# Performance work log

Measured on AMD Instinct MI355X. Metric: run time of the kernel, lower is better.

The kernel has to match this reference:

```python
import jax, jax.numpy as jnp
import numpy as np

N = 100000   # nodes
E = 1600000  # edges (avg degree 16)
D = 64       # feature dim (in_dim)


def setup_inputs() -> dict:
    key = jax.random.key(0)
    k1, k2, k3, k4, k5 = jax.random.split(key, 5)
    h = jax.random.normal(k1, (N, D), dtype=jnp.float32)
    dnorm = jax.random.uniform(k2, (N,), dtype=jnp.float32)  # deg^-1/2 proxy
    # xavier_normal_(gain=1.414) for Linear(2D, 1): std = gain*sqrt(2/(fan_in+fan_out))
    std = 1.414 * np.sqrt(2.0 / (2 * D + 1))
    gate_w = jax.random.normal(k3, (1, 2 * D), dtype=jnp.float32) * std
    gate_b = jnp.zeros((1,), dtype=jnp.float32)
    src = jax.random.randint(k4, (E,), 0, N, dtype=jnp.int32)
    dst = jax.random.randint(k5, (E,), 0, N, dtype=jnp.int32)
    return {"h": h, "dnorm": dnorm, "gate_w": gate_w, "gate_b": gate_b,
            "src": src, "dst": dst}


def reference(h, dnorm, gate_w, gate_b, src, dst):
    # gate(cat[h_dst, h_src]) == h_dst @ W[:, :D].T + h_src @ W[:, D:].T + b
    w_dst = gate_w[0, :D]  # [D]
    w_src = gate_w[0, D:]  # [D]
    h_src = h[src]                                        # [E, D] gather
    g = jnp.tanh(h[dst] @ w_dst + h_src @ w_src + gate_b[0])  # [E]
    e = g * dnorm[dst] * dnorm[src]                       # [E] (dropout p=0 -> identity)
    # u_mul_e + sum: z[v] = sum_{(u->v)} h[u] * e
    z = jax.ops.segment_sum(h_src * e[:, None], dst, num_segments=N)  # [N, D]
    return z
```

## Files before the change

### kernel.cpp

```cpp
#include <hip/hip_runtime.h>
#include <hip/hip_bf16.h>

#define D 64
#define BKT_SHIFT 7
#define BKT_NODES 128
#define NB_CNT 1024
#define DSPLIT_T 1024
#define DSPLIT_E 4096
#define CAP 2560
#define QBINS 512

__device__ __forceinline__ unsigned short f2bf(float x) {
    unsigned u = __float_as_uint(x);
    unsigned r = 0x7fffu + ((u >> 16) & 1u);
    return (unsigned short)((u + r) >> 16);
}

template<bool MAKE_BF16>
__global__ void fal_precompute(const float* __restrict__ h,
                               const float* __restrict__ dnorm,
                               const float* __restrict__ gate_w,
                               const float* __restrict__ gate_b,
                               float2* __restrict__ sd,
                               float2* __restrict__ ss,
                               unsigned short* __restrict__ hb,
                               int* __restrict__ bcursor,
                               int nb, int N) {
    int tid  = threadIdx.x;
    if (blockIdx.x == 0) {
        for (int i = tid; i < nb; i += 256) bcursor[i] = 0;
    }
    int lane = tid & 63;
    int wave = tid >> 6;
    int grp  = lane >> 4;
    int gl   = lane & 15;

    int node = blockIdx.x * 16 + wave * 4 + grp;
    int nc   = node < N ? node : N - 1;

    const float4* h4 = (const float4*)h;
    const float4* w4 = (const float4*)gate_w;

    float4 hv  = h4[nc * 16 + gl];
    float4 wd  = w4[gl];
    float4 wsr = w4[16 + gl];

    if (MAKE_BF16 && node < N) {
        ushort4 p = make_ushort4(f2bf(hv.x), f2bf(hv.y), f2bf(hv.z), f2bf(hv.w));
        *(ushort4*)&hb[(size_t)node * D + gl * 4] = p;
    }

    float a = hv.x * wd.x + hv.y * wd.y + hv.z * wd.z + hv.w * wd.w;
    float b = hv.x * wsr.x + hv.y * wsr.y + hv.z * wsr.z + hv.w * wsr.w;

    for (int off = 1; off < 16; off <<= 1) {
        a += __shfl_xor(a, off, 64);
        b += __shfl_xor(b, off, 64);
    }

    if (gl == 0 && node < N) {
        float dn = dnorm[node];
        sd[node] = make_float2(a + gate_b[0], dn);
        ss[node] = make_float2(b, dn);
    }
}

__global__ __launch_bounds__(DSPLIT_T) void fal_multisplit(
        const int* __restrict__ src,
        const int* __restrict__ dst,
        int* __restrict__ bcursor,
        unsigned* __restrict__ pk_bin,
        int E, int nb) {
    __shared__ int lcount[NB_CNT];
    __shared__ int lscan[NB_CNT];
    __shared__ int gofs[NB_CNT];
    __shared__ int wsum16[16];
    __shared__ unsigned s_pk[DSPLIT_E];
    __shared__ int s_gpos[DSPLIT_E];

    int tid  = threadIdx.x;
    int lane = tid & 63;
    int w    = tid >> 6;
    lcount[tid] = 0;
    __syncthreads();

    int E4 = E >> 2;
    int i4 = blockIdx.x * DSPLIT_T + tid;

    int srcs[4], dsts[4], lr[4];
    bool act = (i4 < E4);
    if (act) {
        int4 s4 = ((const int4*)src)[i4];
        int4 d4 = ((const int4*)dst)[i4];
        srcs[0] = s4.x; srcs[1] = s4.y; srcs[2] = s4.z; srcs[3] = s4.w;
        dsts[0] = d4.x; dsts[1] = d4.y; dsts[2] = d4.z; dsts[3] = d4.w;
        #pragma unroll
        for (int j = 0; j < 4; ++j)
            lr[j] = atomicAdd(&lcount[dsts[j] >> BKT_SHIFT], 1);
    }
    __syncthreads();

    int v = lcount[tid];
    for (int off = 1; off < 64; off <<= 1) {
        int t = __shfl_up(v, off, 64);
        if (lane >= off) v += t;
    }
    if (lane == 63) wsum16[w] = v;
    __syncthreads();
    if (tid < 16) {
        int s = wsum16[tid];
        for (int off = 1; off < 16; off <<= 1) {
            int t = __shfl_up(s, off, 64);
            if (tid >= off) s += t;
        }
        wsum16[tid] = s;
    }
    __syncthreads();
    lscan[tid] = v + (w ? wsum16[w - 1] : 0);

    if (tid < nb) {
        int c = lcount[tid];
        int rel = c ? atomicAdd(&bcursor[tid], c) : 0;
        gofs[tid] = tid * CAP + rel;
    }
    __syncthreads();

    if (act) {
        #pragma unroll
        for (int j = 0; j < 4; ++j) {
            int b = dsts[j] >> BKT_SHIFT;
            int lpos = (lscan[b] - lcount[b]) + lr[j];
            unsigned dl = (unsigned)(dsts[j] & (BKT_NODES - 1));
            s_pk[lpos] = (dl << 20) | (unsigned)srcs[j];
            int gp = gofs[b] + lr[j];
            s_gpos[lpos] = (gp < (b + 1) * CAP) ? gp : -1;
        }
    }
    __syncthreads();

    int total = lscan[NB_CNT - 1];
    for (int t = tid; t < total; t += DSPLIT_T) {
        int g = s_gpos[t];
        if (g >= 0) pk_bin[g] = s_pk[t];
    }
}

#define DRAIN(SEG0, DG, A0, A1, A2, A3, A4, A5, A6, A7) do {             \
    int k_ = 0;                                                          \
    for (; k_ + 2 <= (DG); k_ += 2) {                                    \
        int s0_ = (int)(s_srt[(SEG0) + k_]     & 0xFFFFFu);              \
        int s1_ = (int)(s_srt[(SEG0) + k_ + 1] & 0xFFFFFu);              \
        float e0_ = s_esc[(SEG0) + k_];                                  \
        float e1_ = s_esc[(SEG0) + k_ + 1];                              \
        if constexpr (BF16) {                                            \
            uint4 r0_ = *(const uint4*)&hb[(size_t)s0_ * D + cbase];     \
            uint4 r1_ = *(const uint4*)&hb[(size_t)s1_ * D + cbase];     \
            A0 = fmaf(__uint_as_float(r0_.x << 16),         e0_, A0);    \
            A1 = fmaf(__uint_as_float(r0_.x & 0xffff0000u), e0_, A1);    \
            A2 = fmaf(__uint_as_float(r0_.y << 16),         e0_, A2);    \
            A3 = fmaf(__uint_as_float(r0_.y & 0xffff0000u), e0_, A3);    \
            A4 = fmaf(__uint_as_float(r0_.z << 16),         e0_, A4);    \
            A5 = fmaf(__uint_as_float(r0_.z & 0xffff0000u), e0_, A5);    \
            A6 = fmaf(__uint_as_float(r0_.w << 16),         e0_, A6);    \
            A7 = fmaf(__uint_as_float(r0_.w & 0xffff0000u), e0_, A7);    \
            A0 = fmaf(__uint_as_float(r1_.x << 16),         e1_, A0);    \
            A1 = fmaf(__uint_as_float(r1_.x & 0xffff0000u), e1_, A1);    \
            A2 = fmaf(__uint_as_float(r1_.y << 16),         e1_, A2);    \
            A3 = fmaf(__uint_as_float(r1_.y & 0xffff0000u), e1_, A3);    \
            A4 = fmaf(__uint_as_float(r1_.z << 16),         e1_, A4);    \
            A5 = fmaf(__uint_as_float(r1_.z & 0xffff0000u), e1_, A5);    \
            A6 = fmaf(__uint_as_float(r1_.w << 16),         e1_, A6);    \
            A7 = fmaf(__uint_as_float(r1_.w & 0xffff0000u), e1_, A7);    \
        } else {                                                         \
            const float4* hp0_ = (const float4*)&h[(size_t)s0_ * D + cbase]; \
            const float4* hp1_ = (const float4*)&h[(size_t)s1_ * D + cbase]; \
            float4 q0_ = hp0_[0], q1_ = hp0_[1], q2_ = hp1_[0], q3_ = hp1_[1]; \
            A0 = fmaf(q0_.x, e0_, A0); A1 = fmaf(q0_.y, e0_, A1);        \
            A2 = fmaf(q0_.z, e0_, A2); A3 = fmaf(q0_.w, e0_, A3);        \
            A4 = fmaf(q1_.x, e0_, A4); A5 = fmaf(q1_.y, e0_, A5);        \
            A6 = fmaf(q1_.z, e0_, A6); A7 = fmaf(q1_.w, e0_, A7);        \
            A0 = fmaf(q2_.x, e1_, A0); A1 = fmaf(q2_.y, e1_, A1);        \
            A2 = fmaf(q2_.z, e1_, A2); A3 = fmaf(q2_.w, e1_, A3);        \
            A4 = fmaf(q3_.x, e1_, A4); A5 = fmaf(q3_.y, e1_, A5);        \
            A6 = fmaf(q3_.z, e1_, A6); A7 = fmaf(q3_.w, e1_, A7);        \
        }                                                                \
    }                                                                    \
    if (k_ < (DG)) {                                                     \
        int s0_ = (int)(s_srt[(SEG0) + k_] & 0xFFFFFu);                  \
        float e0_ = s_esc[(SEG0) + k_];                                  \
        if constexpr (BF16) {                                            \
            uint4 r0_ = *(const uint4*)&hb[(size_t)s0_ * D + cbase];     \
            A0 = fmaf(__uint_as_float(r0_.x << 16),         e0_, A0);    \
            A1 = fmaf(__uint_as_float(r0_.x & 0xffff0000u), e0_, A1);    \
            A2 = fmaf(__uint_as_float(r0_.y << 16),         e0_, A2);    \
            A3 = fmaf(__uint_as_float(r0_.y & 0xffff0000u), e0_, A3);    \
            A4 = fmaf(__uint_as_float(r0_.z << 16),         e0_, A4);    \
            A5 = fmaf(__uint_as_float(r0_.z & 0xffff0000u), e0_, A5);    \
            A6 = fmaf(__uint_as_float(r0_.w << 16),         e0_, A6);    \
            A7 = fmaf(__uint_as_float(r0_.w & 0xffff0000u), e0_, A7);    \
        } else {                                                         \
            const float4* hp0_ = (const float4*)&h[(size_t)s0_ * D + cbase]; \
            float4 q0_ = hp0_[0], q1_ = hp0_[1];                         \
            A0 = fmaf(q0_.x, e0_, A0); A1 = fmaf(q0_.y, e0_, A1);        \
            A2 = fmaf(q0_.z, e0_, A2); A3 = fmaf(q0_.w, e0_, A3);        \
            A4 = fmaf(q1_.x, e0_, A4); A5 = fmaf(q1_.y, e0_, A5);        \
            A6 = fmaf(q1_.z, e0_, A6); A7 = fmaf(q1_.w, e0_, A7);        \
        }                                                                \
    }                                                                    \
} while (0)

template<bool BF16>
__global__ __launch_bounds__(512) void fal_bucket_process(
        const float* __restrict__ h,
        const unsigned short* __restrict__ hb,
        const float2* __restrict__ sd,
        const float2* __restrict__ ss,
        const int* __restrict__ bcursor,
        const unsigned* __restrict__ pk_bin,
        float* __restrict__ z, int nfull, int N) {
    __shared__ unsigned s_pk[CAP];
    __shared__ unsigned s_srt[CAP];
    __shared__ float    s_esc[CAP];
    __shared__ float2   sdl[BKT_NODES];
    __shared__ int qhist[QBINS];
    __shared__ int qbase[QBINS];
    __shared__ int qcur[QBINS];
    __shared__ int wsum8[8];

    int bid  = blockIdx.x;
    int tid  = threadIdx.x;
    int lane = tid & 63;
    int w    = tid >> 6;

    int b, h0, is_half;
    if (bid < nfull) { b = bid; h0 = 0; is_half = 0; }
    else {
        int idx = bid - nfull;
        b  = nfull + (idx >> 1);
        h0 = (idx & 1) * 64;
        is_half = 1;
    }

    qhist[tid] = 0;
    if (tid < BKT_NODES) {
        int node = b * BKT_NODES + tid;
        sdl[tid] = (node < N) ? sd[node] : make_float2(0.f, 0.f);
    }
    __syncthreads();

    int cnt = min(bcursor[b], CAP);
    const unsigned* bin = pk_bin + (size_t)b * CAP;

    for (int t = tid; t < cnt; t += 512) {
        unsigned pk = bin[t];
        s_pk[t] = pk;
        int key = (int)(((pk & 0xFFFFFu) >> 15) * 128u + (pk >> 20));
        atomicAdd(&qhist[key], 1);
    }
    __syncthreads();

    int myh = qhist[tid];
    int v = myh;
    for (int off = 1; off < 64; off <<= 1) {
        int t = __shfl_up(v, off, 64);
        if (lane >= off) v += t;
    }
    if (lane == 63) wsum8[w] = v;
    __syncthreads();
    if (tid < 8) {
        int s2 = wsum8[tid];
        for (int off = 1; off < 8; off <<= 1) {
            int t = __shfl_up(s2, off, 64);
            if (tid >= off) s2 += t;
        }
        wsum8[tid] = s2;
    }
    __syncthreads();
    {
        int incl = v + (w ? wsum8[w - 1] : 0);
        qbase[tid] = incl - myh;
        qcur[tid]  = 0;
    }
    __syncthreads();

    for (int t = tid; t < cnt; t += 512) {
        unsigned pk = s_pk[t];
        int dl = (int)(pk >> 20);
        int sn = (int)(pk & 0xFFFFFu);
        int key = (sn >> 15) * 128 + dl;
        int r  = atomicAdd(&qcur[key], 1);
        float2 sv = ss[sn];
        float2 dv = sdl[dl];
        float esc = tanhf(dv.x + sv.x) * dv.y * sv.y;
        int p = qbase[key] + r;
        s_srt[p] = pk;
        s_esc[p] = esc;
    }
    __syncthreads();

    int oct   = tid >> 3;
    int sdim  = tid & 7;
    int cbase = sdim * 8;

    float a0 = 0.f, a1 = 0.f, a2 = 0.f, a3 = 0.f;
    float a4 = 0.f, a5 = 0.f, a6 = 0.f, a7 = 0.f;
    float b0 = 0.f, b1 = 0.f, b2 = 0.f, b3 = 0.f;
    float b4 = 0.f, b5 = 0.f, b6 = 0.f, b7 = 0.f;

    if (!is_half) {
        for (int q = 0; q < 4; ++q) {
            int keyA = q * 128 + oct;
            DRAIN(qbase[keyA], qhist[keyA], a0, a1, a2, a3, a4, a5, a6, a7);
            int keyB = q * 128 + oct + 64;
            DRAIN(qbase[keyB], qhist[keyB], b0, b1, b2, b3, b4, b5, b6, b7);
            __syncthreads();
        }
        int nodeA = b * BKT_NODES + oct;
        if (nodeA < N) {
            float4* zp = (float4*)&z[(size_t)nodeA * D + cbase];
            zp[0] = make_float4(a0, a1, a2, a3);
            zp[1] = make_float4(a4, a5, a6, a7);
        }
        int nodeB = b * BKT_NODES + oct + 64;
        if (nodeB < N) {
            float4* zp = (float4*)&z[(size_t)nodeB * D + cbase];
            zp[0] = make_float4(b0, b1, b2, b3);
            zp[1] = make_float4(b4, b5, b6, b7);
        }
    } else {
        for (int q = 0; q < 4; ++q) {
            int keyA = q * 128 + h0 + oct;
            DRAIN(qbase[keyA], qhist[keyA], a0, a1, a2, a3, a4, a5, a6, a7);
            __syncthreads();
        }
        int nodeA = b * BKT_NODES + h0 + oct;
        if (nodeA < N) {
            float4* zp = (float4*)&z[(size_t)nodeA * D + cbase];
            zp[0] = make_float4(a0, a1, a2, a3);
            zp[1] = make_float4(a4, a5, a6, a7);
        }
    }
}

extern "C" void kernel_launch(void* const* d_in, const int* in_sizes, int n_in,
                              void* d_out, int out_size, void* d_ws, size_t ws_size,
                              hipStream_t stream) {
    const float* h      = (const float*)d_in[0];
    const float* dnorm  = (const float*)d_in[1];
    const float* gate_w = (const float*)d_in[2];
    const float* gate_b = (const float*)d_in[3];
    const int*   src    = (const int*)d_in[4];
    const int*   dst    = (const int*)d_in[5];
    float*       z      = (float*)d_out;

    int N  = in_sizes[1];
    int E  = in_sizes[4];
    int nb = (N + BKT_NODES - 1) >> BKT_SHIFT;

    char* ws0 = (char*)d_ws;
    size_t off = 0;
    auto alloc = [&](size_t bytes) {
        char* p = ws0 + off;
        off += (bytes + 15) & ~(size_t)15;
        return p;
    };
    float2*   sd      = (float2*)alloc((size_t)N * sizeof(float2));
    float2*   ss      = (float2*)alloc((size_t)N * sizeof(float2));
    int*      bcursor = (int*)alloc((size_t)nb * sizeof(int));
    unsigned* pk_bin  = (unsigned*)alloc((size_t)nb * CAP * sizeof(unsigned));
    unsigned short* hb = (unsigned short*)(ws0 + off);
    size_t need_with_hb = off + (size_t)N * D * sizeof(unsigned short);
    bool use_bf16 = (ws_size >= need_with_hb);

    int nfull = nb & ~255;
    int grid3 = nfull + 2 * (nb - nfull);

    if (use_bf16)
        fal_precompute<true><<<(N + 15) / 16, 256, 0, stream>>>(
            h, dnorm, gate_w, gate_b, sd, ss, hb, bcursor, nb, N);
    else
        fal_precompute<false><<<(N + 15) / 16, 256, 0, stream>>>(
            h, dnorm, gate_w, gate_b, sd, ss, hb, bcursor, nb, N);

    fal_multisplit<<<(E + DSPLIT_E - 1) / DSPLIT_E, DSPLIT_T, 0, stream>>>(
        src, dst, bcursor, pk_bin, E, nb);

    if (use_bf16)
        fal_bucket_process<true><<<grid3, 512, 0, stream>>>(
            h, hb, sd, ss, bcursor, pk_bin, z, nfull, N);
    else
        fal_bucket_process<false><<<grid3, 512, 0, stream>>>(
            h, hb, sd, ss, bcursor, pk_bin, z, nfull, N);
}
```

Before: 150.3 us.

## Fuse precompute and multisplit into one launch, drop per-quarter barriers

Merges the per-node gate precompute and the edge bucketing multisplit into a single 1024-thread kernel, with block ranges selecting the role. The bcursor reset moves to a hipMemsetAsync so the split blocks no longer depend on the precompute kernel. This removes one kernel launch and lets both independent stages overlap on the GPU. It also deletes the __syncthreads inside the drain loops of bucket_process, which is only safe if the shared buffers read there are not rewritten between quarters. The precompute blocks now run at 1024 threads and carry the large shared-memory footprint of the split path, which may lower their occupancy.

```diff
diff --git a/kernel.cpp b/kernel.cpp
--- a/kernel.cpp
+++ b/kernel.cpp
@@ -17,131 +17,126 @@
 }
 
 template<bool MAKE_BF16>
-__global__ void fal_precompute(const float* __restrict__ h,
-                               const float* __restrict__ dnorm,
-                               const float* __restrict__ gate_w,
-                               const float* __restrict__ gate_b,
-                               float2* __restrict__ sd,
-                               float2* __restrict__ ss,
-                               unsigned short* __restrict__ hb,
-                               int* __restrict__ bcursor,
-                               int nb, int N) {
-    int tid  = threadIdx.x;
-    if (blockIdx.x == 0) {
-        for (int i = tid; i < nb; i += 256) bcursor[i] = 0;
-    }
-    int lane = tid & 63;
-    int wave = tid >> 6;
-    int grp  = lane >> 4;
-    int gl   = lane & 15;
-
-    int node = blockIdx.x * 16 + wave * 4 + grp;
-    int nc   = node < N ? node : N - 1;
-
-    const float4* h4 = (const float4*)h;
-    const float4* w4 = (const float4*)gate_w;
-
-    float4 hv  = h4[nc * 16 + gl];
-    float4 wd  = w4[gl];
-    float4 wsr = w4[16 + gl];
-
-    if (MAKE_BF16 && node < N) {
-        ushort4 p = make_ushort4(f2bf(hv.x), f2bf(hv.y), f2bf(hv.z), f2bf(hv.w));
-        *(ushort4*)&hb[(size_t)node * D + gl * 4] = p;
-    }
-
-    float a = hv.x * wd.x + hv.y * wd.y + hv.z * wd.z + hv.w * wd.w;
-    float b = hv.x * wsr.x + hv.y * wsr.y + hv.z * wsr.z + hv.w * wsr.w;
-
-    for (int off = 1; off < 16; off <<= 1) {
-        a += __shfl_xor(a, off, 64);
-        b += __shfl_xor(b, off, 64);
-    }
-
-    if (gl == 0 && node < N) {
-        float dn = dnorm[node];
-        sd[node] = make_float2(a + gate_b[0], dn);
-        ss[node] = make_float2(b, dn);
-    }
-}
-
-__global__ __launch_bounds__(DSPLIT_T) void fal_multisplit(
+__global__ __launch_bounds__(1024) void fal_pre_split(
+        const float* __restrict__ h,
+        const float* __restrict__ dnorm,
+        const float* __restrict__ gate_w,
+        const float* __restrict__ gate_b,
+        float2* __restrict__ sd,
+        float2* __restrict__ ss,
+        unsigned short* __restrict__ hb,
         const int* __restrict__ src,
         const int* __restrict__ dst,
         int* __restrict__ bcursor,
         unsigned* __restrict__ pk_bin,
-        int E, int nb) {
-    __shared__ int lcount[NB_CNT];
-    __shared__ int lscan[NB_CNT];
-    __shared__ int gofs[NB_CNT];
-    __shared__ int wsum16[16];
-    __shared__ unsigned s_pk[DSPLIT_E];
-    __shared__ int s_gpos[DSPLIT_E];
-
+        int E, int nb, int N, int gridB) {
     int tid  = threadIdx.x;
     int lane = tid & 63;
     int w    = tid >> 6;
-    lcount[tid] = 0;
-    __syncthreads();
-
-    int E4 = E >> 2;
-    int i4 = blockIdx.x * DSPLIT_T + tid;
-
-    int srcs[4], dsts[4], lr[4];
-    bool act = (i4 < E4);
-    if (act) {
-        int4 s4 = ((const int4*)src)[i4];
-        int4 d4 = ((const int4*)dst)[i4];
-        srcs[0] = s4.x; srcs[1] = s4.y; srcs[2] = s4.z; srcs[3] = s4.w;
-        dsts[0] = d4.x; dsts[1] = d4.y; dsts[2] = d4.z; dsts[3] = d4.w;
-        #pragma unroll
-        for (int j = 0; j < 4; ++j)
-            lr[j] = atomicAdd(&lcount[dsts[j] >> BKT_SHIFT], 1);
-    }
-    __syncthreads();
-
-    int v = lcount[tid];
-    for (int off = 1; off < 64; off <<= 1) {
-        int t = __shfl_up(v, off, 64);
-        if (lane >= off) v += t;
-    }
-    if (lane == 63) wsum16[w] = v;
-    __syncthreads();
-    if (tid < 16) {
-        int s = wsum16[tid];
+
+    if ((int)blockIdx.x < gridB) {
+        __shared__ int lcount[NB_CNT];
+        __shared__ int lscan[NB_CNT];
+        __shared__ int gofs[NB_CNT];
+        __shared__ int wsum16[16];
+        __shared__ unsigned s_pk[DSPLIT_E];
+        __shared__ int s_gpos[DSPLIT_E];
+
+        lcount[tid] = 0;
+        __syncthreads();
+
+        int E4 = E >> 2;
+        int i4 = blockIdx.x * DSPLIT_T + tid;
+
+        int srcs[4], dsts[4], lr[4];
+        bool act = (i4 < E4);
+        if (act) {
+            int4 s4 = ((const int4*)src)[i4];
+            int4 d4 = ((const int4*)dst)[i4];
+            srcs[0] = s4.x; srcs[1] = s4.y; srcs[2] = s4.z; srcs[3] = s4.w;
+            dsts[0] = d4.x; dsts[1] = d4.y; dsts[2] = d4.z; dsts[3] = d4.w;
+            #pragma unroll
+            for (int j = 0; j < 4; ++j)
+                lr[j] = atomicAdd(&lcount[dsts[j] >> BKT_SHIFT], 1);
+        }
+        __syncthreads();
+
+        int v = lcount[tid];
+        for (int off = 1; off < 64; off <<= 1) {
+            int t = __shfl_up(v, off, 64);
+            if (lane >= off) v += t;
+        }
+        if (lane == 63) wsum16[w] = v;
+        __syncthreads();
+        if (tid < 16) {
+            int s = wsum16[tid];
+            for (int off = 1; off < 16; off <<= 1) {
+                int t = __shfl_up(s, off, 64);
+                if (tid >= off) s += t;
+            }
+            wsum16[tid] = s;
+        }
+        __syncthreads();
+        lscan[tid] = v + (w ? wsum16[w - 1] : 0);
+
+        if (tid < nb) {
+            int c = lcount[tid];
+            int rel = c ? atomicAdd(&bcursor[tid], c) : 0;
+            gofs[tid] = tid * CAP + rel;
+        }
+        __syncthreads();
+
+        if (act) {
+            #pragma unroll
+            for (int j = 0; j < 4; ++j) {
+                int b = dsts[j] >> BKT_SHIFT;
+                int lpos = (lscan[b] - lcount[b]) + lr[j];
+                unsigned dl = (unsigned)(dsts[j] & (BKT_NODES - 1));
+                s_pk[lpos] = (dl << 20) | (unsigned)srcs[j];
+                int gp = gofs[b] + lr[j];
+                s_gpos[lpos] = (gp < (b + 1) * CAP) ? gp : -1;
+            }
+        }
+        __syncthreads();
+
+        int total = lscan[NB_CNT - 1];
+        for (int t = tid; t < total; t += DSPLIT_T) {
+            int g = s_gpos[t];
+            if (g >= 0) pk_bin[g] = s_pk[t];
+        }
+    } else {
+        int bid  = blockIdx.x - gridB;
+        int grp  = lane >> 4;
+        int gl   = lane & 15;
+
+        int node = bid * 64 + w * 4 + grp;
+        int nc   = node < N ? node : N - 1;
+
+        const float4* h4 = (const float4*)h;
+        const float4* w4 = (const float4*)gate_w;
+
+        float4 hv  = h4[nc * 16 + gl];
+        float4 wd  = w4[gl];
+        float4 wsr = w4[16 + gl];
+
+        if (MAKE_BF16 && node < N) {
+            ushort4 p = make_ushort4(f2bf(hv.x), f2bf(hv.y), f2bf(hv.z), f2bf(hv.w));
+            *(ushort4*)&hb[(size_t)node * D + gl * 4] = p;
+        }
+
+        float a = hv.x * wd.x + hv.y * wd.y + hv.z * wd.z + hv.w * wd.w;
+        float b = hv.x * wsr.x + hv.y * wsr.y + hv.z * wsr.z + hv.w * wsr.w;
+
         for (int off = 1; off < 16; off <<= 1) {
-            int t = __shfl_up(s, off, 64);
-            if (tid >= off) s += t;
-        }
-        wsum16[tid] = s;
-    }
-    __syncthreads();
-    lscan[tid] = v + (w ? wsum16[w - 1] : 0);
-
-    if (tid < nb) {
-        int c = lcount[tid];
-        int rel = c ? atomicAdd(&bcursor[tid], c) : 0;
-        gofs[tid] = tid * CAP + rel;
-    }
-    __syncthreads();
-
-    if (act) {
-        #pragma unroll
-        for (int j = 0; j < 4; ++j) {
-            int b = dsts[j] >> BKT_SHIFT;
-            int lpos = (lscan[b] - lcount[b]) + lr[j];
-            unsigned dl = (unsigned)(dsts[j] & (BKT_NODES - 1));
-            s_pk[lpos] = (dl << 20) | (unsigned)srcs[j];
-            int gp = gofs[b] + lr[j];
-            s_gpos[lpos] = (gp < (b + 1) * CAP) ? gp : -1;
-        }
-    }
-    __syncthreads();
-
-    int total = lscan[NB_CNT - 1];
-    for (int t = tid; t < total; t += DSPLIT_T) {
-        int g = s_gpos[t];
-        if (g >= 0) pk_bin[g] = s_pk[t];
+            a += __shfl_xor(a, off, 64);
+            b += __shfl_xor(b, off, 64);
+        }
+
+        if (gl == 0 && node < N) {
+            float dn = dnorm[node];
+            sd[node] = make_float2(a + gate_b[0], dn);
+            ss[node] = make_float2(b, dn);
+        }
     }
 }
 
@@ -313,7 +308,6 @@
             DRAIN(qbase[keyA], qhist[keyA], a0, a1, a2, a3, a4, a5, a6, a7);
             int keyB = q * 128 + oct + 64;
             DRAIN(qbase[keyB], qhist[keyB], b0, b1, b2, b3, b4, b5, b6, b7);
-            __syncthreads();
         }
         int nodeA = b * BKT_NODES + oct;
         if (nodeA < N) {
@@ -331,7 +325,6 @@
         for (int q = 0; q < 4; ++q) {
             int keyA = q * 128 + h0 + oct;
             DRAIN(qbase[keyA], qhist[keyA], a0, a1, a2, a3, a4, a5, a6, a7);
-            __syncthreads();
         }
         int nodeA = b * BKT_NODES + h0 + oct;
         if (nodeA < N) {
@@ -372,18 +365,21 @@
     size_t need_with_hb = off + (size_t)N * D * sizeof(unsigned short);
     bool use_bf16 = (ws_size >= need_with_hb);
 
+    int gridB = (E + DSPLIT_E - 1) / DSPLIT_E;
+    int gridA = (N + 63) / 64;
     int nfull = nb & ~255;
     int grid3 = nfull + 2 * (nb - nfull);
 
+    hipMemsetAsync(bcursor, 0, (size_t)nb * sizeof(int), stream);
+
     if (use_bf16)
-        fal_precompute<true><<<(N + 15) / 16, 256, 0, stream>>>(
-            h, dnorm, gate_w, gate_b, sd, ss, hb, bcursor, nb, N);
+        fal_pre_split<true><<<gridB + gridA, 1024, 0, stream>>>(
+            h, dnorm, gate_w, gate_b, sd, ss, hb, src, dst, bcursor, pk_bin,
+            E, nb, N, gridB);
     else
-        fal_precompute<false><<<(N + 15) / 16, 256, 0, stream>>>(
-            h, dnorm, gate_w, gate_b, sd, ss, hb, bcursor, nb, N);
-
-    fal_multisplit<<<(E + DSPLIT_E - 1) / DSPLIT_E, DSPLIT_T, 0, stream>>>(
-        src, dst, bcursor, pk_bin, E, nb);
+        fal_pre_split<false><<<gridB + gridA, 1024, 0, stream>>>(
+            h, dnorm, gate_w, gate_b, sd, ss, hb, src, dst, bcursor, pk_bin,
+            E, nb, N, gridB);
 
     if (use_bf16)
         fal_bucket_process<true><<<grid3, 512, 0, stream>>>(
```

After: 149.7 us. About the same (-0.4%).

## Double edges per multisplit block, split tail buckets into quarters, drop drain syncs

Applied to the files above, without the earlier changes.

The multisplit kernel now handles 8192 edges per block, two int4 loads per thread, which halves the number of blocks and of global bcursor atomics, and makes each bin write burst longer. The shared s_pk/s_gpos arrays grow to 8192 entries, raising LDS use per block and possibly lowering occupancy. Tail buckets in the process kernel are split four ways instead of two, for better load balance on the last partial wave, with only 32 of 64 octets active in those blocks. The __syncthreads inside the drain loops are removed, which looks safe because DRAIN only reads shared data written earlier.

```diff
diff --git a/kernel.cpp b/kernel.cpp
--- a/kernel.cpp
+++ b/kernel.cpp
@@ -6,7 +6,7 @@
 #define BKT_NODES 128
 #define NB_CNT 1024
 #define DSPLIT_T 1024
-#define DSPLIT_E 4096
+#define DSPLIT_E 8192
 #define CAP 2560
 #define QBINS 512
 
@@ -85,19 +85,31 @@
     __syncthreads();
 
     int E4 = E >> 2;
-    int i4 = blockIdx.x * DSPLIT_T + tid;
-
-    int srcs[4], dsts[4], lr[4];
-    bool act = (i4 < E4);
-    if (act) {
-        int4 s4 = ((const int4*)src)[i4];
-        int4 d4 = ((const int4*)dst)[i4];
+    int base4 = blockIdx.x * (DSPLIT_E >> 2);
+    int i4a = base4 + tid;
+    int i4b = base4 + DSPLIT_T + tid;
+
+    int srcs[8], dsts[8], lr[8];
+    bool act_a = (i4a < E4);
+    bool act_b = (i4b < E4);
+    if (act_a) {
+        int4 s4 = ((const int4*)src)[i4a];
+        int4 d4 = ((const int4*)dst)[i4a];
         srcs[0] = s4.x; srcs[1] = s4.y; srcs[2] = s4.z; srcs[3] = s4.w;
         dsts[0] = d4.x; dsts[1] = d4.y; dsts[2] = d4.z; dsts[3] = d4.w;
         #pragma unroll
         for (int j = 0; j < 4; ++j)
             lr[j] = atomicAdd(&lcount[dsts[j] >> BKT_SHIFT], 1);
     }
+    if (act_b) {
+        int4 s4 = ((const int4*)src)[i4b];
+        int4 d4 = ((const int4*)dst)[i4b];
+        srcs[4] = s4.x; srcs[5] = s4.y; srcs[6] = s4.z; srcs[7] = s4.w;
+        dsts[4] = d4.x; dsts[5] = d4.y; dsts[6] = d4.z; dsts[7] = d4.w;
+        #pragma unroll
+        for (int j = 4; j < 8; ++j)
+            lr[j] = atomicAdd(&lcount[dsts[j] >> BKT_SHIFT], 1);
+    }
     __syncthreads();
 
     int v = lcount[tid];
@@ -125,9 +137,20 @@
     }
     __syncthreads();
 
-    if (act) {
+    if (act_a) {
         #pragma unroll
         for (int j = 0; j < 4; ++j) {
+            int b = dsts[j] >> BKT_SHIFT;
+            int lpos = (lscan[b] - lcount[b]) + lr[j];
+            unsigned dl = (unsigned)(dsts[j] & (BKT_NODES - 1));
+            s_pk[lpos] = (dl << 20) | (unsigned)srcs[j];
+            int gp = gofs[b] + lr[j];
+            s_gpos[lpos] = (gp < (b + 1) * CAP) ? gp : -1;
+        }
+    }
+    if (act_b) {
+        #pragma unroll
+        for (int j = 4; j < 8; ++j) {
             int b = dsts[j] >> BKT_SHIFT;
             int lpos = (lscan[b] - lcount[b]) + lr[j];
             unsigned dl = (unsigned)(dsts[j] & (BKT_NODES - 1));
@@ -232,13 +255,13 @@
     int lane = tid & 63;
     int w    = tid >> 6;
 
-    int b, h0, is_half;
-    if (bid < nfull) { b = bid; h0 = 0; is_half = 0; }
+    int b, h0, is_qtr;
+    if (bid < nfull) { b = bid; h0 = 0; is_qtr = 0; }
     else {
         int idx = bid - nfull;
-        b  = nfull + (idx >> 1);
-        h0 = (idx & 1) * 64;
-        is_half = 1;
+        b  = nfull + (idx >> 2);
+        h0 = (idx & 3) * 32;
+        is_qtr = 1;
     }
 
     qhist[tid] = 0;
@@ -307,13 +330,12 @@
     float b0 = 0.f, b1 = 0.f, b2 = 0.f, b3 = 0.f;
     float b4 = 0.f, b5 = 0.f, b6 = 0.f, b7 = 0.f;
 
-    if (!is_half) {
+    if (!is_qtr) {
         for (int q = 0; q < 4; ++q) {
             int keyA = q * 128 + oct;
             DRAIN(qbase[keyA], qhist[keyA], a0, a1, a2, a3, a4, a5, a6, a7);
             int keyB = q * 128 + oct + 64;
             DRAIN(qbase[keyB], qhist[keyB], b0, b1, b2, b3, b4, b5, b6, b7);
-            __syncthreads();
         }
         int nodeA = b * BKT_NODES + oct;
         if (nodeA < N) {
@@ -328,16 +350,17 @@
             zp[1] = make_float4(b4, b5, b6, b7);
         }
     } else {
-        for (int q = 0; q < 4; ++q) {
-            int keyA = q * 128 + h0 + oct;
-            DRAIN(qbase[keyA], qhist[keyA], a0, a1, a2, a3, a4, a5, a6, a7);
-            __syncthreads();
-        }
-        int nodeA = b * BKT_NODES + h0 + oct;
-        if (nodeA < N) {
-            float4* zp = (float4*)&z[(size_t)nodeA * D + cbase];
-            zp[0] = make_float4(a0, a1, a2, a3);
-            zp[1] = make_float4(a4, a5, a6, a7);
+        if (oct < 32) {
+            for (int q = 0; q < 4; ++q) {
+                int keyA = q * 128 + h0 + oct;
+                DRAIN(qbase[keyA], qhist[keyA], a0, a1, a2, a3, a4, a5, a6, a7);
+            }
+            int nodeA = b * BKT_NODES + h0 + oct;
+            if (nodeA < N) {
+                float4* zp = (float4*)&z[(size_t)nodeA * D + cbase];
+                zp[0] = make_float4(a0, a1, a2, a3);
+                zp[1] = make_float4(a4, a5, a6, a7);
+            }
         }
     }
 }
@@ -372,8 +395,9 @@
     size_t need_with_hb = off + (size_t)N * D * sizeof(unsigned short);
     bool use_bf16 = (ws_size >= need_with_hb);
 
+    int grid2 = (E + DSPLIT_E - 1) / DSPLIT_E;
     int nfull = nb & ~255;
-    int grid3 = nfull + 2 * (nb - nfull);
+    int grid3 = nfull + 4 * (nb - nfull);
 
     if (use_bf16)
         fal_precompute<true><<<(N + 15) / 16, 256, 0, stream>>>(
@@ -382,7 +406,7 @@
         fal_precompute<false><<<(N + 15) / 16, 256, 0, stream>>>(
             h, dnorm, gate_w, gate_b, sd, ss, hb, bcursor, nb, N);
 
-    fal_multisplit<<<(E + DSPLIT_E - 1) / DSPLIT_E, DSPLIT_T, 0, stream>>>(
+    fal_multisplit<<<grid2, DSPLIT_T, 0, stream>>>(
         src, dst, bcursor, pk_bin, E, nb);
 
     if (use_bf16)
```

New measurement: 145.5 us. -3.2%, faster.
